# Performance work log

Hardware: AMD Instinct MI355X
Metric: run time of the kernel (lower is better)

## Reference

```python
import jax, jax.numpy as jnp
import numpy as np

GH, GW = 16, 16          # group_size
DIM = 512
H = 8                    # num_heads
PD = DIM // 16           # pos_dim = (dim//4)//4 = 32
B = 256                  # number of groups (batch*windows)
N = GH * GW


def _make_bias_tables():
    # biases buffer: all 2D relative offsets, shape [(2GH-1)*(2GW-1), 2]
    h = np.arange(1 - GH, GH)
    w = np.arange(1 - GW, GW)
    bh, bw = np.meshgrid(h, w, indexing='ij')
    biases = np.stack([bh, bw]).reshape(2, -1).T.astype(np.float32)
    # relative_position_index: [N, N] lookup into the bias table
    ch, cw = np.meshgrid(np.arange(GH), np.arange(GW), indexing='ij')
    coords = np.stack([ch, cw]).reshape(2, -1)            # [2, N]
    rel = coords[:, :, None] - coords[:, None, :]         # [2, N, N]
    rel = rel.transpose(1, 2, 0).copy()                   # [N, N, 2]
    rel[:, :, 0] += GH - 1
    rel[:, :, 1] += GW - 1
    rel[:, :, 0] *= 2 * GW - 1
    idx = rel.sum(-1)
    return biases, idx.astype(np.int32)


def _ln(x, g, b, eps=1e-5):
    m = x.mean(-1, keepdims=True)
    v = ((x - m) ** 2).mean(-1, keepdims=True)
    return (x - m) / jnp.sqrt(v + eps) * g + b


def setup_inputs() -> dict:
    key = jax.random.key(0)
    ks = jax.random.split(key, 16)
    s = 0.02
    biases_np, idx_np = _make_bias_tables()
    return {
        'x': jax.random.normal(ks[0], (B, N, DIM), dtype=jnp.float32),
        'qkv_w': jax.random.normal(ks[1], (DIM, 3 * DIM), dtype=jnp.float32) * s,
        'qkv_b': jnp.zeros((3 * DIM,), jnp.float32),
        'proj_w': jax.random.normal(ks[2], (DIM, DIM), dtype=jnp.float32) * s,
        'proj_b': jnp.zeros((DIM,), jnp.float32),
        'p1_w': jax.random.normal(ks[3], (2, PD), dtype=jnp.float32) * s,
        'p1_b': jnp.zeros((PD,), jnp.float32),
        'g1': jnp.ones((PD,), jnp.float32), 'b1': jnp.zeros((PD,), jnp.float32),
        'p2_w': jax.random.normal(ks[4], (PD, PD), dtype=jnp.float32) * s,
        'p2_b': jnp.zeros((PD,), jnp.float32),
        'g2': jnp.ones((PD,), jnp.float32), 'b2': jnp.zeros((PD,), jnp.float32),
        'p3_w': jax.random.normal(ks[5], (PD, PD), dtype=jnp.float32) * s,
        'p3_b': jnp.zeros((PD,), jnp.float32),
        'g3': jnp.ones((PD,), jnp.float32), 'b3': jnp.zeros((PD,), jnp.float32),
        'p4_w': jax.random.normal(ks[6], (PD, H), dtype=jnp.float32) * s,
        'p4_b': jnp.zeros((H,), jnp.float32),
        'biases': jnp.asarray(biases_np),
        'rel_idx': jnp.asarray(idx_np),
    }


def reference(x, qkv_w, qkv_b, proj_w, proj_b,
              p1_w, p1_b, g1, b1, p2_w, p2_b, g2, b2,
              p3_w, p3_b, g3, b3, p4_w, p4_b, biases, rel_idx):
    Bn, Nn, C = x.shape
    hd = C // H
    scale = hd ** -0.5
    qkv = (x @ qkv_w + qkv_b).reshape(Bn, Nn, 3, H, hd).transpose(2, 0, 3, 1, 4)
    q, k, v = qkv[0] * scale, qkv[1], qkv[2]      # [B, H, N, hd]
    attn = jnp.einsum('bhnd,bhmd->bhnm', q, k)    # [B, H, N, N]
    # dynamic position bias MLP on the offset table
    h1 = jax.nn.relu(_ln(biases @ p1_w + p1_b, g1, b1))
    h2 = jax.nn.relu(_ln(h1 @ p2_w + p2_b, g2, b2))
    h3 = jax.nn.relu(_ln(h2 @ p3_w + p3_b, g3, b3))
    pos = h3 @ p4_w + p4_b                        # [L, H]
    rpb = pos[rel_idx.reshape(-1)].reshape(Nn, Nn, H).transpose(2, 0, 1)  # [H, N, N]
    attn = jax.nn.softmax(attn + rpb[None], axis=-1)
    out = jnp.einsum('bhnm,bhmd->bhnd', attn, v)
    out = out.transpose(0, 2, 1, 3).reshape(Bn, Nn, C)
    return out @ proj_w + proj_b
```

## Files before the change

### kernel.cpp

```cpp
#include <hip/hip_runtime.h>
#include <stdint.h>

typedef __bf16 bf16x8 __attribute__((ext_vector_type(8)));
typedef float  f32x4  __attribute__((ext_vector_type(4)));
typedef unsigned short ushort_t;

#define MFMA16(a,b,c) __builtin_amdgcn_mfma_f32_16x16x32_bf16((a),(b),(c),0,0,0)

#define GLOAD16(gsrc, ldst) \
    __builtin_amdgcn_global_load_lds((const __attribute__((address_space(1))) void*)(gsrc), \
                                     (__attribute__((address_space(3))) void*)(ldst), 16, 0, 0)

#define BATCH 256
#define NTOK  256
#define DIM   512
#define NH    8
#define HD    64
#define PD    32
#define LTAB  961

#define POS_OFF   0
#define RPB_OFF   32768
#define WQKV_OFF  (RPB_OFF + 2097152)
#define WPROJ_OFF (WQKV_OFF + 1572864)
#define QKV_OFF   (WPROJ_OFF + 524288)
#define AOUT_OFF  (QKV_OFF + 201326592)
#define XB_OFF    AOUT_OFF

__device__ __forceinline__ ushort_t f2bf(float f) {
    unsigned int u = __builtin_bit_cast(unsigned int, f);
    u += 0x7FFFu + ((u >> 16) & 1u);
    return (ushort_t)(u >> 16);
}

__global__ __launch_bounds__(256) void convert_x(
    const float* __restrict__ x, ushort_t* __restrict__ xb)
{
    size_t i = ((size_t)blockIdx.x * 256 + threadIdx.x) * 8;
    float4 f0 = *(const float4*)(x + i);
    float4 f1 = *(const float4*)(x + i + 4);
    uint4 o;
    o.x = (unsigned)f2bf(f0.x) | ((unsigned)f2bf(f0.y) << 16);
    o.y = (unsigned)f2bf(f0.z) | ((unsigned)f2bf(f0.w) << 16);
    o.z = (unsigned)f2bf(f1.x) | ((unsigned)f2bf(f1.y) << 16);
    o.w = (unsigned)f2bf(f1.z) | ((unsigned)f2bf(f1.w) << 16);
    *reinterpret_cast<uint4*>(xb + i) = o;
}

__global__ __launch_bounds__(256) void transpose_w(
    const float* __restrict__ src, ushort_t* __restrict__ dst, int K, int Nn)
{
    __shared__ ushort_t tile[64][65];
    int tiles_n = Nn >> 6;
    int tn = blockIdx.x % tiles_n, tk = blockIdx.x / tiles_n;
    int n0 = tn * 64, k0 = tk * 64;
    int t = threadIdx.x;
#pragma unroll
    for (int i = 0; i < 16; i++) {
        int idx = t + i * 256;
        int kl = idx >> 6, nl = idx & 63;
        tile[nl][kl] = f2bf(src[(size_t)(k0 + kl) * Nn + n0 + nl]);
    }
    __syncthreads();
#pragma unroll
    for (int i = 0; i < 16; i++) {
        int idx = t + i * 256;
        int nl = idx >> 6, kl = idx & 63;
        dst[(size_t)(n0 + nl) * K + k0 + kl] = tile[nl][kl];
    }
}

__device__ __forceinline__ float ln_relu_t(float h, int j,
                                           const float* __restrict__ g,
                                           const float* __restrict__ bb) {
    float m = h;
    m += __shfl_xor(m, 1); m += __shfl_xor(m, 2); m += __shfl_xor(m, 4);
    m += __shfl_xor(m, 8); m += __shfl_xor(m, 16);
    m *= (1.0f / PD);
    float d = h - m;
    float v = d * d;
    v += __shfl_xor(v, 1); v += __shfl_xor(v, 2); v += __shfl_xor(v, 4);
    v += __shfl_xor(v, 8); v += __shfl_xor(v, 16);
    v *= (1.0f / PD);
    float x = d * rsqrtf(v + 1e-5f) * g[j] + bb[j];
    return x > 0.f ? x : 0.f;
}

__global__ __launch_bounds__(256) void pos_mlp(
    const float* __restrict__ biases,
    const float* __restrict__ p1_w, const float* __restrict__ p1_b,
    const float* __restrict__ g1, const float* __restrict__ b1,
    const float* __restrict__ p2_w, const float* __restrict__ p2_b,
    const float* __restrict__ g2, const float* __restrict__ b2,
    const float* __restrict__ p3_w, const float* __restrict__ p3_b,
    const float* __restrict__ g3, const float* __restrict__ b3,
    const float* __restrict__ p4_w, const float* __restrict__ p4_b,
    float* __restrict__ pos)
{
    __shared__ float hs[8][33];
    int tid = threadIdx.x;
    int rl = tid >> 5, j = tid & 31;
    int r = blockIdx.x * 8 + rl;
    bool ok = r < LTAB;
    float c0 = ok ? biases[r * 2 + 0] : 0.f;
    float c1 = ok ? biases[r * 2 + 1] : 0.f;

    float h = c0 * p1_w[j] + c1 * p1_w[PD + j] + p1_b[j];
    h = ln_relu_t(h, j, g1, b1);

    hs[rl][j] = h;
    __syncthreads();
    float s = p2_b[j];
#pragma unroll
    for (int i = 0; i < PD; i++) s += hs[rl][i] * p2_w[i * PD + j];
    __syncthreads();
    h = ln_relu_t(s, j, g2, b2);

    hs[rl][j] = h;
    __syncthreads();
    s = p3_b[j];
#pragma unroll
    for (int i = 0; i < PD; i++) s += hs[rl][i] * p3_w[i * PD + j];
    __syncthreads();
    h = ln_relu_t(s, j, g3, b3);

    hs[rl][j] = h;
    __syncthreads();
    if (ok && j < NH) {
        float o = p4_b[j];
#pragma unroll
        for (int i = 0; i < PD; i++) o += hs[rl][i] * p4_w[i * NH + j];
        pos[r * NH + j] = o;
    }
}

__global__ __launch_bounds__(256) void rpb_gather(
    const float* __restrict__ pos, const int* __restrict__ rel_idx,
    float* __restrict__ rpb)
{
    int i = blockIdx.x * 256 + threadIdx.x;
    int idx = rel_idx[i];
#pragma unroll
    for (int hh = 0; hh < NH; hh++) rpb[(size_t)hh * 65536 + i] = pos[idx * NH + hh];
}

__global__ __launch_bounds__(512, 1) void qkv_gemm(
    const ushort_t* __restrict__ xb, const ushort_t* __restrict__ wT,
    const float* __restrict__ qkv_b, ushort_t* __restrict__ qkvb)
{
    __shared__ ushort_t As[2][256 * 64];
    __shared__ ushort_t Bs[2][256 * 64];
    int t = threadIdx.x;
    int bid = blockIdx.x;
    int wgid = (bid & 7) * 192 + (bid >> 3);
    int mt = wgid / 6, nt = wgid % 6;
    int m0 = mt * 256, n0 = nt * 256;
    int lane = t & 63, w = t >> 6;
    int wm = w >> 2, wn = w & 3;
    int lr = lane & 15, lk = lane >> 4;
    int srow8 = lane >> 3;
    int sch = ((lane & 7) ^ srow8) * 8;
    const ushort_t* Asrc = xb + (size_t)(m0 + srow8) * 512 + sch;
    const ushort_t* Bsrc = wT + (size_t)(n0 + srow8) * 512 + sch;
    int arw = w & 3;
    int ch0 = ((lk) ^ (lr & 7)) * 8;
    int ch1 = ((4 + lk) ^ (lr & 7)) * 8;
    int arow = wm * 128 + lr;
    int brow = wn * 64 + lr;

    f32x4 acc[8][4];
#pragma unroll
    for (int fr = 0; fr < 8; fr++)
#pragma unroll
        for (int fc = 0; fc < 4; fc++) acc[fr][fc] = (f32x4){0.f, 0.f, 0.f, 0.f};

#define QSTAGE(buf, kt) do { \
    if (w < 4) { \
        _Pragma("unroll") \
        for (int i_ = 0; i_ < 8; i_++) { \
            int rb_ = arw * 64 + i_ * 8; \
            GLOAD16(Asrc + (size_t)rb_ * 512 + (kt) * 64, &As[buf][rb_ * 64]); \
        } \
    } else { \
        _Pragma("unroll") \
        for (int i_ = 0; i_ < 8; i_++) { \
            int rb_ = arw * 64 + i_ * 8; \
            GLOAD16(Bsrc + (size_t)rb_ * 512 + (kt) * 64, &Bs[buf][rb_ * 64]); \
        } \
    } } while (0)

    QSTAGE(0, 0);
    asm volatile("s_waitcnt vmcnt(0)" ::: "memory");
    __syncthreads();
    for (int kt = 0; kt < 8; ++kt) {
        int cb = kt & 1;
        if (kt < 7) QSTAGE(cb ^ 1, kt + 1);
#pragma unroll
        for (int kh = 0; kh < 2; kh++) {
            int ch = kh ? ch1 : ch0;
            bf16x8 a[8], b[4];
#pragma unroll
            for (int fr = 0; fr < 8; fr++)
                a[fr] = *reinterpret_cast<const bf16x8*>(&As[cb][(arow + fr * 16) * 64 + ch]);
#pragma unroll
            for (int fc = 0; fc < 4; fc++)
                b[fc] = *reinterpret_cast<const bf16x8*>(&Bs[cb][(brow + fc * 16) * 64 + ch]);
#pragma unroll
            for (int fr = 0; fr < 8; fr++)
#pragma unroll
                for (int fc = 0; fc < 4; fc++)
                    acc[fr][fc] = MFMA16(a[fr], b[fc], acc[fr][fc]);
        }
        if (kt < 7) {
            asm volatile("s_waitcnt vmcnt(0)" ::: "memory");
            __syncthreads();
        }
    }
#undef QSTAGE

    int s = n0 >> 9;
    int bg = m0 >> 8;
    if (s < 2) {
        float sc = (s == 0) ? 0.125f : 1.0f;
#pragma unroll
        for (int fc = 0; fc < 4; fc++) {
            int n = n0 + wn * 64 + fc * 16 + lr;
            float bias = qkv_b[n];
            int hh = (n >> 6) & 7, d = n & 63;
            ushort_t* dst = qkvb + ((((size_t)s * 256 + bg) * 8 + hh) * 256) * 64 + d;
#pragma unroll
            for (int fr = 0; fr < 8; fr++)
#pragma unroll
                for (int r = 0; r < 4; r++) {
                    int tok = wm * 128 + fr * 16 + lk * 4 + r;
                    dst[(size_t)tok * 64] = f2bf((acc[fr][fc][r] + bias) * sc);
                }
        }
    } else {
#pragma unroll
        for (int fc = 0; fc < 4; fc++) {
            int n = n0 + wn * 64 + fc * 16 + lr;
            float bias = qkv_b[n];
            int hh = (n >> 6) & 7, d = n & 63;
            ushort_t* dst = qkvb + ((((size_t)512 + bg) * 8 + hh) * 64 + d) * 256;
#pragma unroll
            for (int fr = 0; fr < 8; fr++) {
                int tok = wm * 128 + fr * 16 + lk * 4;
                uint2 pk;
                pk.x = (unsigned)f2bf(acc[fr][fc][0] + bias) |
                       ((unsigned)f2bf(acc[fr][fc][1] + bias) << 16);
                pk.y = (unsigned)f2bf(acc[fr][fc][2] + bias) |
                       ((unsigned)f2bf(acc[fr][fc][3] + bias) << 16);
                *reinterpret_cast<uint2*>(dst + tok) = pk;
            }
        }
    }
}

__global__ __launch_bounds__(256) void attn_kernel(
    const ushort_t* __restrict__ qkvb, const float* __restrict__ rpb,
    ushort_t* __restrict__ aout)
{
    __shared__ ushort_t Ps[4][32][40];
    __shared__ ushort_t Os[4][16 * 72];
    int t = threadIdx.x, lane = t & 63, w = t >> 6;
    int bid = blockIdx.x;
    int qh = bid & 1; int bh = bid >> 1; int hh = bh & 7; int bg = bh >> 3;
    const ushort_t* Qg  = qkvb + (((size_t)bg * 8 + hh) * 256) * 64;
    const ushort_t* Kg  = qkvb + (((size_t)(256 + bg) * 8 + hh) * 256) * 64;
    const ushort_t* VTg = qkvb + (((size_t)(512 + bg) * 8 + hh) * 64) * 256;
    int lr = lane & 15, lk = lane >> 4;
    int qrow0 = qh * 128 + w * 32;

    bf16x8 qf[2][2];
#pragma unroll
    for (int fr = 0; fr < 2; fr++)
#pragma unroll
        for (int kc = 0; kc < 2; kc++)
            qf[fr][kc] = *reinterpret_cast<const bf16x8*>(
                Qg + (size_t)(qrow0 + fr * 16 + lr) * 64 + kc * 32 + lk * 8);

    f32x4 oacc[2][4];
    float rsumq[2] = {0.f, 0.f};
#pragma unroll
    for (int fr = 0; fr < 2; fr++)
#pragma unroll
        for (int fc = 0; fc < 4; fc++) oacc[fr][fc] = (f32x4){0.f, 0.f, 0.f, 0.f};

    const float* rpbh = rpb + (size_t)hh * 65536;

    for (int kt = 0; kt < 8; ++kt) {
        f32x4 sacc[2][2];
#pragma unroll
        for (int fk = 0; fk < 2; fk++)
#pragma unroll
            for (int fq = 0; fq < 2; fq++) sacc[fk][fq] = (f32x4){0.f, 0.f, 0.f, 0.f};
#pragma unroll
        for (int kc = 0; kc < 2; kc++) {
            bf16x8 kb0 = *reinterpret_cast<const bf16x8*>(
                Kg + (size_t)(kt * 32 + lr) * 64 + kc * 32 + lk * 8);
            bf16x8 kb1 = *reinterpret_cast<const bf16x8*>(
                Kg + (size_t)(kt * 32 + 16 + lr) * 64 + kc * 32 + lk * 8);
            sacc[0][0] = MFMA16(kb0, qf[0][kc], sacc[0][0]);
            sacc[0][1] = MFMA16(kb0, qf[1][kc], sacc[0][1]);
            sacc[1][0] = MFMA16(kb1, qf[0][kc], sacc[1][0]);
            sacc[1][1] = MFMA16(kb1, qf[1][kc], sacc[1][1]);
        }
#pragma unroll
        for (int fq = 0; fq < 2; fq++) {
            int q = qrow0 + fq * 16 + lr;
#pragma unroll
            for (int fk = 0; fk < 2; fk++) {
                int kcol = kt * 32 + fk * 16 + lk * 4;
                const float4 rv = *reinterpret_cast<const float4*>(
                    rpbh + (size_t)q * 256 + kcol);
                float p0 = __expf(sacc[fk][fq][0] + rv.x);
                float p1 = __expf(sacc[fk][fq][1] + rv.y);
                float p2 = __expf(sacc[fk][fq][2] + rv.z);
                float p3 = __expf(sacc[fk][fq][3] + rv.w);
                rsumq[fq] += (p0 + p1) + (p2 + p3);
                uint2 pk;
                pk.x = (unsigned)f2bf(p0) | ((unsigned)f2bf(p1) << 16);
                pk.y = (unsigned)f2bf(p2) | ((unsigned)f2bf(p3) << 16);
                *reinterpret_cast<uint2*>(&Ps[w][fq * 16 + lr][fk * 16 + lk * 4]) = pk;
            }
        }
        bf16x8 pa[2], vb[4];
#pragma unroll
        for (int fr = 0; fr < 2; fr++)
            pa[fr] = *reinterpret_cast<const bf16x8*>(&Ps[w][fr * 16 + lr][lk * 8]);
#pragma unroll
        for (int fc = 0; fc < 4; fc++)
            vb[fc] = *reinterpret_cast<const bf16x8*>(
                VTg + (size_t)(fc * 16 + lr) * 256 + kt * 32 + lk * 8);
#pragma unroll
        for (int fr = 0; fr < 2; fr++)
#pragma unroll
            for (int fc = 0; fc < 4; fc++)
                oacc[fr][fc] = MFMA16(pa[fr], vb[fc], oacc[fr][fc]);
    }
#pragma unroll
    for (int fq = 0; fq < 2; fq++) {
        float s = rsumq[fq];
        s += __shfl_xor(s, 16); s += __shfl_xor(s, 32);
        rsumq[fq] = __frcp_rn(s);
    }
    float rinv[2][4];
#pragma unroll
    for (int fr = 0; fr < 2; fr++)
#pragma unroll
        for (int r = 0; r < 4; r++)
            rinv[fr][r] = __shfl(rsumq[fr], lk * 4 + r);

#pragma unroll
    for (int fr = 0; fr < 2; fr++) {
#pragma unroll
        for (int fc = 0; fc < 4; fc++)
#pragma unroll
            for (int r = 0; r < 4; r++)
                Os[w][(lk * 4 + r) * 72 + fc * 16 + lr] = f2bf(oacc[fr][fc][r] * rinv[fr][r]);
#pragma unroll
        for (int ii = 0; ii < 2; ii++) {
            int j = lane + ii * 64;
            int row = j >> 3, ch = j & 7;
            uint4 v = *reinterpret_cast<const uint4*>(&Os[w][row * 72 + ch * 8]);
            *reinterpret_cast<uint4*>(
                aout + ((size_t)(bg * 256 + qrow0 + fr * 16 + row)) * 512 + hh * 64 + ch * 8) = v;
        }
    }
}

__global__ __launch_bounds__(512, 1) void proj_gemm(
    const ushort_t* __restrict__ ain, const ushort_t* __restrict__ wT,
    const float* __restrict__ proj_b, float* __restrict__ out)
{
    __shared__ ushort_t As[2][256 * 64];
    __shared__ ushort_t Bs[2][256 * 64];
    int t = threadIdx.x;
    int bid = blockIdx.x;
    int wgid = (bid & 7) * 64 + (bid >> 3);
    int mt = wgid / 2, nt = wgid % 2;
    int m0 = mt * 256, n0 = nt * 256;
    int lane = t & 63, w = t >> 6;
    int wm = w >> 2, wn = w & 3;
    int lr = lane & 15, lk = lane >> 4;
    int srow8 = lane >> 3;
    int sch = ((lane & 7) ^ srow8) * 8;
    const ushort_t* Asrc = ain + (size_t)(m0 + srow8) * 512 + sch;
    const ushort_t* Bsrc = wT + (size_t)(n0 + srow8) * 512 + sch;
    int arw = w & 3;
    int ch0 = ((lk) ^ (lr & 7)) * 8;
    int ch1 = ((4 + lk) ^ (lr & 7)) * 8;
    int arow = wm * 128 + lr;
    int brow = wn * 64 + lr;

    f32x4 acc[8][4];
#pragma unroll
    for (int fr = 0; fr < 8; fr++)
#pragma unroll
        for (int fc = 0; fc < 4; fc++) acc[fr][fc] = (f32x4){0.f, 0.f, 0.f, 0.f};

#define PSTAGE(buf, kt) do { \
    if (w < 4) { \
        _Pragma("unroll") \
        for (int i_ = 0; i_ < 8; i_++) { \
            int rb_ = arw * 64 + i_ * 8; \
            GLOAD16(Asrc + (size_t)rb_ * 512 + (kt) * 64, &As[buf][rb_ * 64]); \
        } \
    } else { \
        _Pragma("unroll") \
        for (int i_ = 0; i_ < 8; i_++) { \
            int rb_ = arw * 64 + i_ * 8; \
            GLOAD16(Bsrc + (size_t)rb_ * 512 + (kt) * 64, &Bs[buf][rb_ * 64]); \
        } \
    } } while (0)

    PSTAGE(0, 0);
    asm volatile("s_waitcnt vmcnt(0)" ::: "memory");
    __syncthreads();
    for (int kt = 0; kt < 8; ++kt) {
        int cb = kt & 1;
        if (kt < 7) PSTAGE(cb ^ 1, kt + 1);
#pragma unroll
        for (int kh = 0; kh < 2; kh++) {
            int ch = kh ? ch1 : ch0;
            bf16x8 a[8], b[4];
#pragma unroll
            for (int fr = 0; fr < 8; fr++)
                a[fr] = *reinterpret_cast<const bf16x8*>(&As[cb][(arow + fr * 16) * 64 + ch]);
#pragma unroll
            for (int fc = 0; fc < 4; fc++)
                b[fc] = *reinterpret_cast<const bf16x8*>(&Bs[cb][(brow + fc * 16) * 64 + ch]);
#pragma unroll
            for (int fr = 0; fr < 8; fr++)
#pragma unroll
                for (int fc = 0; fc < 4; fc++)
                    acc[fr][fc] = MFMA16(a[fr], b[fc], acc[fr][fc]);
        }
        if (kt < 7) {
            asm volatile("s_waitcnt vmcnt(0)" ::: "memory");
            __syncthreads();
        }
    }
#undef PSTAGE
#pragma unroll
    for (int fc = 0; fc < 4; fc++) {
        int n = n0 + wn * 64 + fc * 16 + lr;
        float bias = proj_b[n];
#pragma unroll
        for (int fr = 0; fr < 8; fr++)
#pragma unroll
            for (int r = 0; r < 4; r++) {
                int m = m0 + wm * 128 + fr * 16 + lk * 4 + r;
                out[(size_t)m * 512 + n] = acc[fr][fc][r] + bias;
            }
    }
}

extern "C" void kernel_launch(void* const* d_in, const int* in_sizes, int n_in,
                              void* d_out, int out_size, void* d_ws, size_t ws_size,
                              hipStream_t stream) {
    const float* x      = (const float*)d_in[0];
    const float* qkv_w  = (const float*)d_in[1];
    const float* qkv_b  = (const float*)d_in[2];
    const float* proj_w = (const float*)d_in[3];
    const float* proj_b = (const float*)d_in[4];
    const float* p1_w = (const float*)d_in[5];
    const float* p1_b = (const float*)d_in[6];
    const float* g1   = (const float*)d_in[7];
    const float* b1   = (const float*)d_in[8];
    const float* p2_w = (const float*)d_in[9];
    const float* p2_b = (const float*)d_in[10];
    const float* g2   = (const float*)d_in[11];
    const float* b2   = (const float*)d_in[12];
    const float* p3_w = (const float*)d_in[13];
    const float* p3_b = (const float*)d_in[14];
    const float* g3   = (const float*)d_in[15];
    const float* b3   = (const float*)d_in[16];
    const float* p4_w = (const float*)d_in[17];
    const float* p4_b = (const float*)d_in[18];
    const float* biases  = (const float*)d_in[19];
    const int*   rel_idx = (const int*)d_in[20];
    float* out = (float*)d_out;

    char* ws = (char*)d_ws;
    float*    pos    = (float*)(ws + POS_OFF);
    float*    rpb    = (float*)(ws + RPB_OFF);
    ushort_t* wqkvT  = (ushort_t*)(ws + WQKV_OFF);
    ushort_t* wprojT = (ushort_t*)(ws + WPROJ_OFF);
    ushort_t* qkvb   = (ushort_t*)(ws + QKV_OFF);
    ushort_t* aoutb  = (ushort_t*)(ws + AOUT_OFF);
    ushort_t* xb     = (ushort_t*)(ws + XB_OFF);

    convert_x<<<dim3(16384), dim3(256), 0, stream>>>(x, xb);
    transpose_w<<<dim3(24 * 8), dim3(256), 0, stream>>>(qkv_w, wqkvT, 512, 1536);
    transpose_w<<<dim3(8 * 8), dim3(256), 0, stream>>>(proj_w, wprojT, 512, 512);
    pos_mlp<<<dim3(121), dim3(256), 0, stream>>>(biases, p1_w, p1_b, g1, b1,
                                                 p2_w, p2_b, g2, b2,
                                                 p3_w, p3_b, g3, b3,
                                                 p4_w, p4_b, pos);
    rpb_gather<<<dim3(256), dim3(256), 0, stream>>>(pos, rel_idx, rpb);
    qkv_gemm<<<dim3(1536), dim3(512), 0, stream>>>(xb, wqkvT, qkv_b, qkvb);
    attn_kernel<<<dim3(4096), dim3(256), 0, stream>>>(qkvb, rpb, aoutb);
    proj_gemm<<<dim3(512), dim3(512), 0, stream>>>(aoutb, wprojT, proj_b, out);
}
```

Measured before the change: 415.5 us.

## Prefetch K tiles and issue rpb/V loads early; one block per head-group

The attention kernel now runs one 512-thread block per (group, head) covering all 256 query rows, instead of two 256-thread blocks. The block index is remapped so consecutive blocks share a head, which should improve L2 reuse of the rpb table. K fragments are double-buffered in registers with a one-tile prefetch, and the rpb and V loads are issued at the top of each iteration to hide global-memory latency behind the MFMAs. The cost is higher register pressure and more shared memory per block, which may lower occupancy.

```diff
diff --git a/kernel.cpp b/kernel.cpp
--- a/kernel.cpp
+++ b/kernel.cpp
@@ -257,20 +257,21 @@
     }
 }
 
-__global__ __launch_bounds__(256) void attn_kernel(
+__global__ __launch_bounds__(512) void attn_kernel(
     const ushort_t* __restrict__ qkvb, const float* __restrict__ rpb,
     ushort_t* __restrict__ aout)
 {
-    __shared__ ushort_t Ps[4][32][40];
-    __shared__ ushort_t Os[4][16 * 72];
+    __shared__ ushort_t Ps[8][32][40];
+    __shared__ ushort_t Os[8][16 * 72];
     int t = threadIdx.x, lane = t & 63, w = t >> 6;
     int bid = blockIdx.x;
-    int qh = bid & 1; int bh = bid >> 1; int hh = bh & 7; int bg = bh >> 3;
+    int wgid = (bid & 7) * 256 + (bid >> 3);
+    int hh = wgid >> 8, bg = wgid & 255;
     const ushort_t* Qg  = qkvb + (((size_t)bg * 8 + hh) * 256) * 64;
     const ushort_t* Kg  = qkvb + (((size_t)(256 + bg) * 8 + hh) * 256) * 64;
     const ushort_t* VTg = qkvb + (((size_t)(512 + bg) * 8 + hh) * 64) * 256;
     int lr = lane & 15, lk = lane >> 4;
-    int qrow0 = qh * 128 + w * 32;
+    int qrow0 = w * 32;
 
     bf16x8 qf[2][2];
 #pragma unroll
@@ -289,7 +290,38 @@
 
     const float* rpbh = rpb + (size_t)hh * 65536;
 
+    bf16x8 kb[2][2][2];
+#pragma unroll
+    for (int kc = 0; kc < 2; kc++)
+#pragma unroll
+        for (int h = 0; h < 2; h++)
+            kb[0][kc][h] = *reinterpret_cast<const bf16x8*>(
+                Kg + (size_t)(h * 16 + lr) * 64 + kc * 32 + lk * 8);
+
+#pragma unroll
     for (int kt = 0; kt < 8; ++kt) {
+        const int cur = kt & 1, nxt = cur ^ 1;
+        if (kt < 7) {
+#pragma unroll
+            for (int kc = 0; kc < 2; kc++)
+#pragma unroll
+                for (int h = 0; h < 2; h++)
+                    kb[nxt][kc][h] = *reinterpret_cast<const bf16x8*>(
+                        Kg + (size_t)((kt + 1) * 32 + h * 16 + lr) * 64 + kc * 32 + lk * 8);
+        }
+        float4 rv[2][2];
+#pragma unroll
+        for (int fq = 0; fq < 2; fq++)
+#pragma unroll
+            for (int fk = 0; fk < 2; fk++)
+                rv[fq][fk] = *reinterpret_cast<const float4*>(
+                    rpbh + (size_t)(qrow0 + fq * 16 + lr) * 256 + kt * 32 + fk * 16 + lk * 4);
+        bf16x8 vb[4];
+#pragma unroll
+        for (int fc = 0; fc < 4; fc++)
+            vb[fc] = *reinterpret_cast<const bf16x8*>(
+                VTg + (size_t)(fc * 16 + lr) * 256 + kt * 32 + lk * 8);
+
         f32x4 sacc[2][2];
 #pragma unroll
         for (int fk = 0; fk < 2; fk++)
@@ -297,27 +329,19 @@
             for (int fq = 0; fq < 2; fq++) sacc[fk][fq] = (f32x4){0.f, 0.f, 0.f, 0.f};
 #pragma unroll
         for (int kc = 0; kc < 2; kc++) {
-            bf16x8 kb0 = *reinterpret_cast<const bf16x8*>(
-                Kg + (size_t)(kt * 32 + lr) * 64 + kc * 32 + lk * 8);
-            bf16x8 kb1 = *reinterpret_cast<const bf16x8*>(
-                Kg + (size_t)(kt * 32 + 16 + lr) * 64 + kc * 32 + lk * 8);
-            sacc[0][0] = MFMA16(kb0, qf[0][kc], sacc[0][0]);
-            sacc[0][1] = MFMA16(kb0, qf[1][kc], sacc[0][1]);
-            sacc[1][0] = MFMA16(kb1, qf[0][kc], sacc[1][0]);
-            sacc[1][1] = MFMA16(kb1, qf[1][kc], sacc[1][1]);
+            sacc[0][0] = MFMA16(kb[cur][kc][0], qf[0][kc], sacc[0][0]);
+            sacc[0][1] = MFMA16(kb[cur][kc][0], qf[1][kc], sacc[0][1]);
+            sacc[1][0] = MFMA16(kb[cur][kc][1], qf[0][kc], sacc[1][0]);
+            sacc[1][1] = MFMA16(kb[cur][kc][1], qf[1][kc], sacc[1][1]);
         }
 #pragma unroll
         for (int fq = 0; fq < 2; fq++) {
-            int q = qrow0 + fq * 16 + lr;
 #pragma unroll
             for (int fk = 0; fk < 2; fk++) {
-                int kcol = kt * 32 + fk * 16 + lk * 4;
-                const float4 rv = *reinterpret_cast<const float4*>(
-                    rpbh + (size_t)q * 256 + kcol);
-                float p0 = __expf(sacc[fk][fq][0] + rv.x);
-                float p1 = __expf(sacc[fk][fq][1] + rv.y);
-                float p2 = __expf(sacc[fk][fq][2] + rv.z);
-                float p3 = __expf(sacc[fk][fq][3] + rv.w);
+                float p0 = __expf(sacc[fk][fq][0] + rv[fq][fk].x);
+                float p1 = __expf(sacc[fk][fq][1] + rv[fq][fk].y);
+                float p2 = __expf(sacc[fk][fq][2] + rv[fq][fk].z);
+                float p3 = __expf(sacc[fk][fq][3] + rv[fq][fk].w);
                 rsumq[fq] += (p0 + p1) + (p2 + p3);
                 uint2 pk;
                 pk.x = (unsigned)f2bf(p0) | ((unsigned)f2bf(p1) << 16);
@@ -325,14 +349,10 @@
                 *reinterpret_cast<uint2*>(&Ps[w][fq * 16 + lr][fk * 16 + lk * 4]) = pk;
             }
         }
-        bf16x8 pa[2], vb[4];
+        bf16x8 pa[2];
 #pragma unroll
         for (int fr = 0; fr < 2; fr++)
             pa[fr] = *reinterpret_cast<const bf16x8*>(&Ps[w][fr * 16 + lr][lk * 8]);
-#pragma unroll
-        for (int fc = 0; fc < 4; fc++)
-            vb[fc] = *reinterpret_cast<const bf16x8*>(
-                VTg + (size_t)(fc * 16 + lr) * 256 + kt * 32 + lk * 8);
 #pragma unroll
         for (int fr = 0; fr < 2; fr++)
 #pragma unroll
@@ -501,6 +521,6 @@
                                                  p4_w, p4_b, pos);
     rpb_gather<<<dim3(256), dim3(256), 0, stream>>>(pos, rel_idx, rpb);
     qkv_gemm<<<dim3(1536), dim3(512), 0, stream>>>(xb, wqkvT, qkv_b, qkvb);
-    attn_kernel<<<dim3(4096), dim3(256), 0, stream>>>(qkvb, rpb, aoutb);
+    attn_kernel<<<dim3(2048), dim3(512), 0, stream>>>(qkvb, rpb, aoutb);
     proj_gemm<<<dim3(512), dim3(512), 0, stream>>>(aoutb, wprojT, proj_b, out);
 }
```

After: 428.3 us. +3.1%, slower.
